# Kernel tuning notes

Hardware: AMD Instinct MI355X
Metric: run time of the kernel (lower is better)

## Reference

```python
import jax, jax.numpy as jnp
import numpy as np

B = 4096
N = 8192
LEVEL_SIZES = [8, 128, 2048, 6008]  # sums to N; 4-level taxonomy
EPS = 1e-07


def _build_hierarchy():
    """parent[c] = parent node index (-1 for roots); level_of[c] = depth."""
    rng = np.random.default_rng(0)
    parent = np.full(N, -1, np.int32)
    level_of = np.zeros(N, np.int32)
    off, prev_start, prev_size = 0, 0, 0
    for l, sz in enumerate(LEVEL_SIZES):
        level_of[off:off + sz] = l
        if l > 0:
            parent[off:off + sz] = rng.integers(prev_start, prev_start + prev_size, sz)
        prev_start, prev_size = off, sz
        off += sz
    return parent, level_of


def setup_inputs() -> dict:
    key = jax.random.key(0)
    k1, k2 = jax.random.split(key)
    pred = jax.random.normal(k1, (B, N), dtype=jnp.float32)  # logits
    target = (jax.random.uniform(k2, (B, N)) < 0.02).astype(jnp.float32)
    parent_np, level_np = _build_hierarchy()
    return {
        "pred": pred,
        "target": target,
        "parent": jnp.asarray(parent_np),
        "level_of": jnp.asarray(level_np),
        "mode": 0,  # 0 = EVAL (propagate conditional probs), 1 = TRAIN
    }


def reference(pred, target, parent, level_of, mode):
    p = jax.nn.sigmoid(pred)                      # [B, N]
    parent_clip = jnp.maximum(parent, 0)          # safe gather index for roots
    is_root = parent < 0                          # recursive_relation[-1]

    if mode != 1:  # not 'TRAIN': top-down conditional probability propagation
        pc = p
        for l in range(1, len(LEVEL_SIZES)):
            # pred_clone[:, children(n)] = pred[:, children] * pred_clone[:, n]
            pc = jnp.where(level_of == l, p * pc[:, parent_clip], pc)
        pred_clone = pc
    else:
        pred_clone = None

    # mask[b, c] = 1 if c is a root, or if target[b, parent[c]] == 1
    mask = jnp.where(is_root, jnp.float32(1.0), target[:, parent_clip])

    pcl = jnp.clip(p, EPS, 1.0 - EPS)
    loss = -(jnp.log(pcl) * target + (1.0 - target) * mask * jnp.log(1.0 - pcl))
    loss = loss.sum(axis=1).mean()
    return (loss, pred_clone)
```

## Files before the change

### kernel.cpp

```cpp
#include <hip/hip_runtime.h>


#define N_NODES 8192
#define L1S 8
#define L2S 136
#define L3S 2184
#define N4   (N_NODES / 4)
#define L3S4 (L3S / 4)

__device__ __forceinline__ float frcp(float x) { return __builtin_amdgcn_rcpf(x); }

__global__ __launch_bounds__(256) void cs_main(
    const float* __restrict__ pred,
    const float* __restrict__ target,
    const int* __restrict__ parent,
    float* __restrict__ out,
    float* __restrict__ bsum,
    float inv_b)
{
    __shared__ float pk[L3S];
    __shared__ float red[4];

    const int tid = threadIdx.x;
    const int b = blockIdx.x;
    const float* __restrict__ prow = pred + (size_t)b * N_NODES;
    const float* __restrict__ trow = target + (size_t)b * N_NODES;
    float* __restrict__ orow = out + 1 + (size_t)b * N_NODES;

    float lsum = 0.0f;

    for (int c4 = tid; c4 < L3S4; c4 += 256) {
        const float4 x4 = ((const float4*)prow)[c4];
        const float4 t4 = ((const float4*)trow)[c4];
        const float xs[4] = {x4.x, x4.y, x4.z, x4.w};
        const float ts[4] = {t4.x, t4.y, t4.z, t4.w};
        const int c0 = c4 * 4;
#pragma unroll
        for (int j = 0; j < 4; ++j) {
            const float p = frcp(1.0f + __expf(-xs[j]));
            pk[c0 + j] = ts[j] > 0.5f ? -p : p;
        }
    }
    __syncthreads();

    for (int c = tid; c < L3S; c += 256) {
        const float v = pk[c];
        const float p = fabsf(v);
        const float t = (v < 0.0f) ? 1.0f : 0.0f;
        float mask, cum;
        if (c < L1S) {
            mask = 1.0f; cum = p;
        } else if (c < L2S) {
            const float pv = pk[parent[c]];
            mask = (pv < 0.0f) ? 1.0f : 0.0f;
            cum = p * fabsf(pv);
        } else {
            const int pa = parent[c];
            const float pv = pk[pa];
            const float gv = pk[parent[pa]];
            mask = (pv < 0.0f) ? 1.0f : 0.0f;
            cum = p * fabsf(pv) * fabsf(gv);
            pk[c] = (t > 0.0f) ? -cum : cum;
        }
        lsum += t * (-__logf(p)) + (1.0f - t) * mask * (-__logf(1.0f - p));
        orow[c] = cum;
    }
    __syncthreads();

    auto proc = [&](int g, const float4& x4, const float4& t4, const int4& q4) {
        const float xs[4] = {x4.x, x4.y, x4.z, x4.w};
        const float ts[4] = {t4.x, t4.y, t4.z, t4.w};
        const int   qs[4] = {q4.x, q4.y, q4.z, q4.w};
        float r[4];
#pragma unroll
        for (int j = 0; j < 4; ++j) {
            const float x = xs[j], t = ts[j];
            const float pv = pk[qs[j]];
            const float mask = (pv < 0.0f) ? 1.0f : 0.0f;
            const float e = __expf(-x);
            const float s = __logf(1.0f + e);
            const float p = frcp(1.0f + e);
            lsum += t * s + (1.0f - t) * mask * (s + x);
            r[j] = p * fabsf(pv);
        }
        const int c0 = g * 4;
        orow[c0] = r[0];
        *(float2*)(orow + c0 + 1) = make_float2(r[1], r[2]);
        orow[c0 + 3] = r[3];
    };

    for (int g0 = L3S4 + tid; g0 < N4; g0 += 512) {
        const int g1 = g0 + 256;
        const float4 xa = ((const float4*)prow)[g0];
        const float4 ta = ((const float4*)trow)[g0];
        const int4  qa = ((const int4*)parent)[g0];
        const bool hb = (g1 < N4);
        float4 xb, tb; int4 qb;
        if (hb) {
            xb = ((const float4*)prow)[g1];
            tb = ((const float4*)trow)[g1];
            qb = ((const int4*)parent)[g1];
        }
        proc(g0, xa, ta, qa);
        if (hb) proc(g1, xb, tb, qb);
    }

#pragma unroll
    for (int off = 32; off > 0; off >>= 1) lsum += __shfl_down(lsum, off);
    if ((tid & 63) == 0) red[tid >> 6] = lsum;
    __syncthreads();
    if (tid == 0) {
        const float s = (red[0] + red[1]) + (red[2] + red[3]);
        if (bsum) bsum[blockIdx.x] = s;
        else atomicAdd(out, s * inv_b);
    }
}

__global__ __launch_bounds__(256) void cs_finish(
    const float* __restrict__ bsum, float* __restrict__ out,
    int nblocks, float inv_b)
{
    __shared__ float red[4];
    const int tid = threadIdx.x;
    float s = 0.0f;
    for (int i = tid; i < nblocks; i += 256) s += bsum[i];
#pragma unroll
    for (int off = 32; off > 0; off >>= 1) s += __shfl_down(s, off);
    if ((tid & 63) == 0) red[tid >> 6] = s;
    __syncthreads();
    if (tid == 0) out[0] = ((red[0] + red[1]) + (red[2] + red[3])) * inv_b;
}

extern "C" void kernel_launch(void* const* d_in, const int* in_sizes, int n_in,
                              void* d_out, int out_size, void* d_ws, size_t ws_size,
                              hipStream_t stream) {
    const float* pred   = (const float*)d_in[0];
    const float* target = (const float*)d_in[1];
    const int*   parent = (const int*)d_in[2];

    float* out = (float*)d_out;
    const int batch = in_sizes[0] / N_NODES;
    const float inv_b = 1.0f / (float)batch;

    if (ws_size >= (size_t)batch * sizeof(float)) {
        float* bsum = (float*)d_ws;
        cs_main<<<batch, 256, 0, stream>>>(pred, target, parent, out, bsum, inv_b);
        cs_finish<<<1, 256, 0, stream>>>(bsum, out, batch, inv_b);
    } else {
        hipMemsetAsync(d_out, 0, sizeof(float), stream);
        cs_main<<<batch, 256, 0, stream>>>(pred, target, parent, out, nullptr, inv_b);
    }
}
```

Before: 92.10 us.

## Prefetch whole row into registers upfront and preload parent indices

```diff
diff --git a/kernel.cpp b/kernel.cpp
--- a/kernel.cpp
+++ b/kernel.cpp
@@ -7,10 +7,13 @@
 #define L3S 2184
 #define N4   (N_NODES / 4)
 #define L3S4 (L3S / 4)
+#define NA 3
+#define NB 6
+#define NF 9
 
 __device__ __forceinline__ float frcp(float x) { return __builtin_amdgcn_rcpf(x); }
 
-__global__ __launch_bounds__(256) void cs_main(
+__global__ __launch_bounds__(256, 4) void cs_main(
     const float* __restrict__ pred,
     const float* __restrict__ target,
     const int* __restrict__ parent,
@@ -27,82 +30,101 @@
     const float* __restrict__ trow = target + (size_t)b * N_NODES;
     float* __restrict__ orow = out + 1 + (size_t)b * N_NODES;
 
+    float4 ax[NA], atg[NA];
+#pragma unroll
+    for (int k = 0; k < NA; ++k) {
+        const int g = min(tid + k * 256, L3S4 - 1);
+        ax[k]  = ((const float4*)prow)[g];
+        atg[k] = ((const float4*)trow)[g];
+    }
+    float4 bx[NB], btg[NB]; int4 bq[NB];
+#pragma unroll
+    for (int k = 0; k < NB; ++k) {
+        const int g = min(L3S4 + tid + k * 256, N4 - 1);
+        bx[k]  = ((const float4*)prow)[g];
+        btg[k] = ((const float4*)trow)[g];
+        bq[k]  = ((const int4*)parent)[g];
+    }
+
+#pragma unroll
+    for (int k = 0; k < NA; ++k) {
+        const int g = tid + k * 256;
+        if (g < L3S4) {
+            const float xs[4] = {ax[k].x, ax[k].y, ax[k].z, ax[k].w};
+            const float ts[4] = {atg[k].x, atg[k].y, atg[k].z, atg[k].w};
+            const int c0 = g * 4;
+#pragma unroll
+            for (int j = 0; j < 4; ++j) {
+                const float p = frcp(1.0f + __expf(-xs[j]));
+                pk[c0 + j] = ts[j] > 0.5f ? -p : p;
+            }
+        }
+    }
+
+    int q1[NF], q2[NF];
+#pragma unroll
+    for (int k = 0; k < NF; ++k) {
+        const int c = min(tid + k * 256, L3S - 1);
+        q1[k] = parent[c];
+    }
+#pragma unroll
+    for (int k = 0; k < NF; ++k) {
+        q2[k] = parent[max(q1[k], 0)];
+    }
+    __syncthreads();
+
     float lsum = 0.0f;
-
-    for (int c4 = tid; c4 < L3S4; c4 += 256) {
-        const float4 x4 = ((const float4*)prow)[c4];
-        const float4 t4 = ((const float4*)trow)[c4];
-        const float xs[4] = {x4.x, x4.y, x4.z, x4.w};
-        const float ts[4] = {t4.x, t4.y, t4.z, t4.w};
-        const int c0 = c4 * 4;
 #pragma unroll
-        for (int j = 0; j < 4; ++j) {
-            const float p = frcp(1.0f + __expf(-xs[j]));
-            pk[c0 + j] = ts[j] > 0.5f ? -p : p;
+    for (int k = 0; k < NF; ++k) {
+        const int c = tid + k * 256;
+        if (c < L3S) {
+            const float v = pk[c];
+            const float p = fabsf(v);
+            const bool t = (v < 0.0f);
+            float mask, cum;
+            if (c < L1S) {
+                mask = 1.0f; cum = p;
+            } else {
+                const float pv = pk[q1[k]];
+                mask = (pv < 0.0f) ? 1.0f : 0.0f;
+                if (c < L2S) {
+                    cum = p * fabsf(pv);
+                } else {
+                    const float gv = pk[q2[k]];
+                    cum = p * fabsf(pv) * fabsf(gv);
+                    pk[c] = t ? -cum : cum;
+                }
+            }
+            lsum += t ? -__logf(p) : mask * (-__logf(1.0f - p));
+            orow[c] = cum;
         }
     }
     __syncthreads();
 
-    for (int c = tid; c < L3S; c += 256) {
-        const float v = pk[c];
-        const float p = fabsf(v);
-        const float t = (v < 0.0f) ? 1.0f : 0.0f;
-        float mask, cum;
-        if (c < L1S) {
-            mask = 1.0f; cum = p;
-        } else if (c < L2S) {
-            const float pv = pk[parent[c]];
-            mask = (pv < 0.0f) ? 1.0f : 0.0f;
-            cum = p * fabsf(pv);
-        } else {
-            const int pa = parent[c];
-            const float pv = pk[pa];
-            const float gv = pk[parent[pa]];
-            mask = (pv < 0.0f) ? 1.0f : 0.0f;
-            cum = p * fabsf(pv) * fabsf(gv);
-            pk[c] = (t > 0.0f) ? -cum : cum;
+#pragma unroll
+    for (int k = 0; k < NB; ++k) {
+        const int g = L3S4 + tid + k * 256;
+        if (g < N4) {
+            const float xs[4] = {bx[k].x, bx[k].y, bx[k].z, bx[k].w};
+            const float ts[4] = {btg[k].x, btg[k].y, btg[k].z, btg[k].w};
+            const int   qs[4] = {bq[k].x, bq[k].y, bq[k].z, bq[k].w};
+            float r[4];
+#pragma unroll
+            for (int j = 0; j < 4; ++j) {
+                const float x = xs[j], t = ts[j];
+                const float pv = pk[qs[j]];
+                const float mask = (pv < 0.0f) ? 1.0f : 0.0f;
+                const float e = __expf(-x);
+                const float s = __logf(1.0f + e);
+                const float p = frcp(1.0f + e);
+                lsum += t * s + (1.0f - t) * mask * (s + x);
+                r[j] = p * fabsf(pv);
+            }
+            const int c0 = g * 4;
+            orow[c0] = r[0];
+            *(float2*)(orow + c0 + 1) = make_float2(r[1], r[2]);
+            orow[c0 + 3] = r[3];
         }
-        lsum += t * (-__logf(p)) + (1.0f - t) * mask * (-__logf(1.0f - p));
-        orow[c] = cum;
-    }
-    __syncthreads();
-
-    auto proc = [&](int g, const float4& x4, const float4& t4, const int4& q4) {
-        const float xs[4] = {x4.x, x4.y, x4.z, x4.w};
-        const float ts[4] = {t4.x, t4.y, t4.z, t4.w};
-        const int   qs[4] = {q4.x, q4.y, q4.z, q4.w};
-        float r[4];
-#pragma unroll
-        for (int j = 0; j < 4; ++j) {
-            const float x = xs[j], t = ts[j];
-            const float pv = pk[qs[j]];
-            const float mask = (pv < 0.0f) ? 1.0f : 0.0f;
-            const float e = __expf(-x);
-            const float s = __logf(1.0f + e);
-            const float p = frcp(1.0f + e);
-            lsum += t * s + (1.0f - t) * mask * (s + x);
-            r[j] = p * fabsf(pv);
-        }
-        const int c0 = g * 4;
-        orow[c0] = r[0];
-        *(float2*)(orow + c0 + 1) = make_float2(r[1], r[2]);
-        orow[c0 + 3] = r[3];
-    };
-
-    for (int g0 = L3S4 + tid; g0 < N4; g0 += 512) {
-        const int g1 = g0 + 256;
-        const float4 xa = ((const float4*)prow)[g0];
-        const float4 ta = ((const float4*)trow)[g0];
-        const int4  qa = ((const int4*)parent)[g0];
-        const bool hb = (g1 < N4);
-        float4 xb, tb; int4 qb;
-        if (hb) {
-            xb = ((const float4*)prow)[g1];
-            tb = ((const float4*)trow)[g1];
-            qb = ((const int4*)parent)[g1];
-        }
-        proc(g0, xa, ta, qa);
-        if (hb) proc(g1, xb, tb, qb);
     }
 
 #pragma unroll
```

Measured after the change: 89.02 us. 3.3% less time.
